# Kernel optimization log

Measured on AMD Instinct MI355X. Metric: run time of the kernel, lower is better.

## Reference

```python
import jax, jax.numpy as jnp
import numpy as np

N_NODES = 50000
N_EDGES = 800000
D_IN = 256
D_HID = 256
D_OUT = 256


def setup_inputs() -> dict:
    key = jax.random.key(0)
    ks = jax.random.split(key, 14)
    s = 1.0 / np.sqrt(D_IN)
    inp = {
        "x": jax.random.normal(ks[0], (N_NODES, D_IN), dtype=jnp.float32),
        "edge_index": jax.random.randint(ks[1], (2, N_EDGES), 0, N_NODES, dtype=jnp.int64),
        "edge_attr": jax.random.uniform(ks[2], (N_EDGES, 1), dtype=jnp.float32),
        # GCNConv layer weights (3 layers)
        "W1": jax.random.normal(ks[3], (D_IN, D_HID), dtype=jnp.float32) * s,
        "b1": jnp.zeros((D_HID,), dtype=jnp.float32),
        "W2": jax.random.normal(ks[4], (D_HID, D_HID), dtype=jnp.float32) * s,
        "b2": jnp.zeros((D_HID,), dtype=jnp.float32),
        "W3": jax.random.normal(ks[5], (D_HID, D_OUT), dtype=jnp.float32) * s,
        "b3": jnp.zeros((D_OUT,), dtype=jnp.float32),
        # edge MLP: Linear(1,8) -> ReLU -> Linear(8,1) -> Sigmoid
        "mw1": jax.random.normal(ks[6], (1, 8), dtype=jnp.float32),
        "mb1": jnp.zeros((8,), dtype=jnp.float32),
        "mw2": jax.random.normal(ks[7], (8, 1), dtype=jnp.float32) * (1.0 / np.sqrt(8.0)),
        "mb2": jnp.zeros((1,), dtype=jnp.float32),
    }
    return inp


def _gcn_layer(x, src, dst, ew, W, b, n):
    """PyG GCNConv: add self-loops (weight 1), symmetric normalization."""
    deg = jax.ops.segment_sum(ew, dst, num_segments=n) + 1.0  # self-loop contributes 1
    dinv = jax.lax.rsqrt(deg)                                 # [N]
    norm = dinv[src] * ew * dinv[dst]                         # [E]
    h = x @ W + b                                             # [N, d_out]
    agg = jax.ops.segment_sum(h[src] * norm[:, None], dst, num_segments=n)
    # self-loop term: dinv[i] * 1 * dinv[i] = 1/deg[i]
    return agg + h * (1.0 / deg)[:, None]


def reference(x, edge_index, edge_attr, W1, b1, W2, b2, W3, b3, mw1, mb1, mw2, mb2):
    src, dst = edge_index[0], edge_index[1]
    # edge weight MLP with sigmoid gate
    h = jax.nn.relu(edge_attr @ mw1 + mb1)
    ew = jax.nn.sigmoid(h @ mw2 + mb2)[:, 0]  # [E]

    n = x.shape[0]
    x = jax.nn.relu(_gcn_layer(x, src, dst, ew, W1, b1, n))  # dropout inactive (eval)
    x = jax.nn.relu(_gcn_layer(x, src, dst, ew, W2, b2, n))
    x = _gcn_layer(x, src, dst, ew, W3, b3, n)
    return x
```

## Files before the change

kernel.cpp:

```cpp
#include <hip/hip_runtime.h>
#include <hip/hip_bf16.h>
#include <stdint.h>

#define GCN_N 50000
#define GCN_E 800000
#define GCN_D 256

typedef __attribute__((ext_vector_type(8))) short bf16x8;
typedef __attribute__((ext_vector_type(4))) float f32x4;
typedef unsigned short ushort_t;
typedef unsigned long long u64;

__device__ __forceinline__ float bf2f(ushort_t u) {
    return __uint_as_float(((unsigned)u) << 16);
}
__device__ __forceinline__ ushort_t f2bf(float f) {
    unsigned v = __float_as_uint(f);
    v += 0x7FFFu + ((v >> 16) & 1u);
    return (ushort_t)(v >> 16);
}


__global__ void init_kernel(u64* dc, int n) {
    int i = blockIdx.x * blockDim.x + threadIdx.x;
    if (i < n) dc[i] = 0ull;
}

__global__ void edge_mlp_kernel(const float* __restrict__ attr,
                                const int* __restrict__ dst,
                                const float* __restrict__ mw1, const float* __restrict__ mb1,
                                const float* __restrict__ mw2, const float* __restrict__ mb2,
                                float* __restrict__ ew, u64* __restrict__ dc,
                                int* __restrict__ rank, int e_count) {
    int e = blockIdx.x * blockDim.x + threadIdx.x;
    if (e >= e_count) return;
    float a = attr[e];
    float s = mb2[0];
#pragma unroll
    for (int j = 0; j < 8; ++j) {
        float hj = fmaf(a, mw1[j], mb1[j]);
        hj = fmaxf(hj, 0.0f);
        s = fmaf(hj, mw2[j], s);
    }
    float w = 1.0f / (1.0f + expf(-s));
    ew[e] = w;
    u64 pack = (1ull << 40) + (u64)((double)w * 4294967296.0);
    u64 old = atomicAdd(&dc[dst[e]], pack);
    rank[e] = (int)(old >> 40);
}

__global__ void node_kernel(const u64* __restrict__ dc, float* __restrict__ dinv,
                            float* __restrict__ invdeg, int n) {
    int i = blockIdx.x * blockDim.x + threadIdx.x;
    if (i < n) {
        u64 v = dc[i];
        float wsum = (float)((double)(v & ((1ull << 40) - 1)) * (1.0 / 4294967296.0));
        float d = 1.0f + wsum;
        dinv[i] = rsqrtf(d);
        invdeg[i] = 1.0f / d;
    }
}

__global__ __launch_bounds__(1024) void scan1_kernel(const u64* __restrict__ dc,
                                                     int* __restrict__ part,
                                                     int* __restrict__ bsum, int n) {
    __shared__ int s[1024];
    int tid = threadIdx.x;
    int i = blockIdx.x * 1024 + tid;
    int v = (i < n) ? (int)(dc[i] >> 40) : 0;
    s[tid] = v;
    __syncthreads();
#pragma unroll
    for (int d = 1; d < 1024; d <<= 1) {
        int t = (tid >= d) ? s[tid - d] : 0;
        __syncthreads();
        s[tid] += t;
        __syncthreads();
    }
    if (i < n) part[i] = s[tid] - v;
    if (tid == 1023) bsum[blockIdx.x] = s[1023];
}

__global__ void scan2_kernel(int* bsum, int nb) {
    int t = threadIdx.x;
    int orig = (t < nb) ? bsum[t] : 0;
    int v = orig;
#pragma unroll
    for (int d = 1; d < 64; d <<= 1) {
        int u = __shfl_up(v, d, 64);
        if (t >= d) v += u;
    }
    if (t < nb) bsum[t] = v - orig;
}

__global__ void scan3_kernel(const int* __restrict__ part, const int* __restrict__ bsum,
                             int* __restrict__ offs, int n, int e_total) {
    int i = blockIdx.x * blockDim.x + threadIdx.x;
    if (i < n) offs[i] = part[i] + bsum[i >> 10];
    if (i == 0) offs[n] = e_total;
}

__global__ void scatter_kernel(const int* __restrict__ src, const int* __restrict__ dst,
                               const float* __restrict__ ew, const float* __restrict__ dinv,
                               const int* __restrict__ offs, const int* __restrict__ rank,
                               int2* __restrict__ csr, int e_count) {
    int e = blockIdx.x * blockDim.x + threadIdx.x;
    if (e >= e_count) return;
    int sN = src[e], dN = dst[e];
    int pos = offs[dN] + rank[e];
    float w = dinv[sN] * ew[e] * dinv[dN];
    csr[pos] = make_int2(sN, __float_as_int(w));
}


__global__ __launch_bounds__(256) void wconvert_kernel(const float* __restrict__ W,
                                                       ushort_t* __restrict__ wtf_hi,
                                                       ushort_t* __restrict__ wtf_lo) {
    __shared__ ushort_t lds_hi[32][256];
    __shared__ ushort_t lds_lo[32][256];
    const int kt = blockIdx.x;
    const int tid = threadIdx.x;
    for (int c = 0; c < 32; ++c) {
        float f = W[(kt * 32 + c) * GCN_D + tid];
        unsigned u = __float_as_uint(f);
        ushort_t hi = (ushort_t)(u >> 16);
        float r = f - __uint_as_float(u & 0xFFFF0000u);
        lds_hi[c][tid] = hi;
        lds_lo[c][tid] = f2bf(r);
    }
    __syncthreads();
#pragma unroll
    for (int q = 0; q < 4; ++q) {
        int slot = q * 256 + tid;
        int lane = slot & 63, nt = slot >> 6;
        int n = nt * 16 + (lane & 15);
        int kl = (lane >> 4) * 8;
        ushort_t h8[8], l8[8];
#pragma unroll
        for (int j = 0; j < 8; ++j) { h8[j] = lds_hi[kl + j][n]; l8[j] = lds_lo[kl + j][n]; }
        size_t o = ((size_t)(kt * 16 + nt) * 64 + lane) * 8;
#pragma unroll
        for (int j = 0; j < 8; ++j) { wtf_hi[o + j] = h8[j]; wtf_lo[o + j] = l8[j]; }
    }
}


__device__ __forceinline__ void split_f32x8(float4 f0, float4 f1, bf16x8& hi, bf16x8& lo) {
    float f[8] = {f0.x, f0.y, f0.z, f0.w, f1.x, f1.y, f1.z, f1.w};
#pragma unroll
    for (int i = 0; i < 8; ++i) {
        unsigned u = __float_as_uint(f[i]);
        hi[i] = (short)(u >> 16);
        float r = f[i] - __uint_as_float(u & 0xFFFF0000u);
        lo[i] = (short)f2bf(r);
    }
}

__global__ __launch_bounds__(256) void mfma_gemm_f32_kernel(
        const float* __restrict__ x,
        const ushort_t* __restrict__ wtf_hi,
        const ushort_t* __restrict__ wtf_lo,
        const float* __restrict__ bias,
        ushort_t* __restrict__ out_h,
        int n_rows) {
    __shared__ ushort_t csmem[4 * 16 * 132];
    const int lane = threadIdx.x & 63;
    const int wv   = threadIdx.x >> 6;
    const int r16  = lane & 15;
    const int kg   = lane >> 4;
    const int row0 = blockIdx.x * 32 + (wv >> 1) * 16;
    const int nt0  = (wv & 1) * 8;

    f32x4 acc[8];
#pragma unroll
    for (int nt = 0; nt < 8; ++nt) acc[nt] = (f32x4){0.f, 0.f, 0.f, 0.f};

    const int arow = row0 + r16;
    const float* ap = (arow < n_rows) ? &x[(size_t)arow * GCN_D + kg * 8] : nullptr;

#pragma unroll 1
    for (int kt = 0; kt < 8; ++kt) {
        float4 f0 = make_float4(0.f, 0.f, 0.f, 0.f), f1 = f0;
        if (ap) {
            f0 = *(const float4*)(ap + kt * 32);
            f1 = *(const float4*)(ap + kt * 32 + 4);
        }
        const bf16x8* bhp = (const bf16x8*)wtf_hi + ((size_t)kt * 16 + nt0) * 64 + lane;
        const bf16x8* blp = (const bf16x8*)wtf_lo + ((size_t)kt * 16 + nt0) * 64 + lane;
        bf16x8 bh[8], bl[8];
#pragma unroll
        for (int nt = 0; nt < 8; ++nt) bh[nt] = bhp[nt * 64];
#pragma unroll
        for (int nt = 0; nt < 8; ++nt) bl[nt] = blp[nt * 64];
        bf16x8 a_hi, a_lo;
        split_f32x8(f0, f1, a_hi, a_lo);
#pragma unroll
        for (int nt = 0; nt < 8; ++nt) {
            acc[nt] = __builtin_amdgcn_mfma_f32_16x16x32_bf16(a_hi, bh[nt], acc[nt], 0, 0, 0);
            acc[nt] = __builtin_amdgcn_mfma_f32_16x16x32_bf16(a_lo, bh[nt], acc[nt], 0, 0, 0);
            acc[nt] = __builtin_amdgcn_mfma_f32_16x16x32_bf16(a_hi, bl[nt], acc[nt], 0, 0, 0);
        }
    }

    ushort_t* my = csmem + wv * (16 * 132);
#pragma unroll
    for (int nt = 0; nt < 8; ++nt) {
        float bv = bias[(nt0 + nt) * 16 + r16];
#pragma unroll
        for (int r = 0; r < 4; ++r)
            my[(kg * 4 + r) * 132 + nt * 16 + r16] = f2bf(acc[nt][r] + bv);
    }
#pragma unroll 4
    for (int r = 0; r < 16; ++r) {
        int row = row0 + r;
        if (row < n_rows) {
            unsigned v = *(unsigned*)&my[r * 132 + lane * 2];
            *(unsigned*)&out_h[(size_t)row * GCN_D + nt0 * 16 + lane * 2] = v;
        }
    }
}


__global__ __launch_bounds__(256) void mfma_gemm_bf16_kernel(
        const ushort_t* __restrict__ a_in,
        const ushort_t* __restrict__ wtf_hi,
        const float* __restrict__ bias,
        ushort_t* __restrict__ out_h,
        int n_rows) {
    __shared__ ushort_t csmem[4 * 16 * 132];
    const int lane = threadIdx.x & 63;
    const int wv   = threadIdx.x >> 6;
    const int r16  = lane & 15;
    const int kg   = lane >> 4;
    const int row0 = blockIdx.x * 32 + (wv >> 1) * 16;
    const int nt0  = (wv & 1) * 8;

    f32x4 acc[8];
#pragma unroll
    for (int nt = 0; nt < 8; ++nt) acc[nt] = (f32x4){0.f, 0.f, 0.f, 0.f};

    const int arow = row0 + r16;
    const ushort_t* ap = (arow < n_rows) ? &a_in[(size_t)arow * GCN_D + kg * 8] : nullptr;

#pragma unroll 2
    for (int kt = 0; kt < 8; ++kt) {
        bf16x8 a = (bf16x8){0, 0, 0, 0, 0, 0, 0, 0};
        if (ap) a = *(const bf16x8*)(ap + kt * 32);
        const bf16x8* bhp = (const bf16x8*)wtf_hi + ((size_t)kt * 16 + nt0) * 64 + lane;
        bf16x8 bh[8];
#pragma unroll
        for (int nt = 0; nt < 8; ++nt) bh[nt] = bhp[nt * 64];
#pragma unroll
        for (int nt = 0; nt < 8; ++nt)
            acc[nt] = __builtin_amdgcn_mfma_f32_16x16x32_bf16(a, bh[nt], acc[nt], 0, 0, 0);
    }

    ushort_t* my = csmem + wv * (16 * 132);
#pragma unroll
    for (int nt = 0; nt < 8; ++nt) {
        float bv = bias[(nt0 + nt) * 16 + r16];
#pragma unroll
        for (int r = 0; r < 4; ++r)
            my[(kg * 4 + r) * 132 + nt * 16 + r16] = f2bf(acc[nt][r] + bv);
    }
#pragma unroll 4
    for (int r = 0; r < 16; ++r) {
        int row = row0 + r;
        if (row < n_rows) {
            unsigned v = *(unsigned*)&my[r * 132 + lane * 2];
            *(unsigned*)&out_h[(size_t)row * GCN_D + nt0 * 16 + lane * 2] = v;
        }
    }
}


template <int OUT_BF16>
__global__ __launch_bounds__(256) void spmm_kernel(const ushort_t* __restrict__ h,
                                                   const int* __restrict__ offs,
                                                   const int2* __restrict__ csr,
                                                   const float* __restrict__ invdeg,
                                                   void* __restrict__ outp, int n) {
    int wid = (blockIdx.x * blockDim.x + threadIdx.x) >> 6;
    int lane = threadIdx.x & 63;
    if (wid >= n) return;
    const ushort4* h4 = (const ushort4*)h;
    ushort4 sv = h4[(size_t)wid * 64 + lane];
    float sw = invdeg[wid];
    float4 acc;
    acc.x = bf2f(sv.x) * sw; acc.y = bf2f(sv.y) * sw;
    acc.z = bf2f(sv.z) * sw; acc.w = bf2f(sv.w) * sw;
    int e0 = offs[wid], e1 = offs[wid + 1];
    int k = e0;
    for (; k + 16 <= e1; k += 16) {
        int2 ee[16]; ushort4 vv[16];
#pragma unroll
        for (int u = 0; u < 16; ++u) ee[u] = csr[k + u];
#pragma unroll
        for (int u = 0; u < 16; ++u) vv[u] = h4[(size_t)ee[u].x * 64 + lane];
#pragma unroll
        for (int u = 0; u < 16; ++u) {
            float w = __int_as_float(ee[u].y);
            acc.x = fmaf(w, bf2f(vv[u].x), acc.x);
            acc.y = fmaf(w, bf2f(vv[u].y), acc.y);
            acc.z = fmaf(w, bf2f(vv[u].z), acc.z);
            acc.w = fmaf(w, bf2f(vv[u].w), acc.w);
        }
    }
    if (k + 8 <= e1) {
        int2 ee[8]; ushort4 vv[8];
#pragma unroll
        for (int u = 0; u < 8; ++u) ee[u] = csr[k + u];
#pragma unroll
        for (int u = 0; u < 8; ++u) vv[u] = h4[(size_t)ee[u].x * 64 + lane];
#pragma unroll
        for (int u = 0; u < 8; ++u) {
            float w = __int_as_float(ee[u].y);
            acc.x = fmaf(w, bf2f(vv[u].x), acc.x);
            acc.y = fmaf(w, bf2f(vv[u].y), acc.y);
            acc.z = fmaf(w, bf2f(vv[u].z), acc.z);
            acc.w = fmaf(w, bf2f(vv[u].w), acc.w);
        }
        k += 8;
    }
    for (; k < e1; ++k) {
        int2 e = csr[k];
        float w = __int_as_float(e.y);
        ushort4 hv = h4[(size_t)e.x * 64 + lane];
        acc.x = fmaf(w, bf2f(hv.x), acc.x);
        acc.y = fmaf(w, bf2f(hv.y), acc.y);
        acc.z = fmaf(w, bf2f(hv.z), acc.z);
        acc.w = fmaf(w, bf2f(hv.w), acc.w);
    }
    if (OUT_BF16) {
        ushort4 o;
        o.x = f2bf(fmaxf(acc.x, 0.f));
        o.y = f2bf(fmaxf(acc.y, 0.f));
        o.z = f2bf(fmaxf(acc.z, 0.f));
        o.w = f2bf(fmaxf(acc.w, 0.f));
        ((ushort4*)outp)[(size_t)wid * 64 + lane] = o;
    } else {
        ((float4*)outp)[(size_t)wid * 64 + lane] = acc;
    }
}


extern "C" void kernel_launch(void* const* d_in, const int* in_sizes, int n_in,
                              void* d_out, int out_size, void* d_ws, size_t ws_size,
                              hipStream_t stream) {
    const float* x    = (const float*)d_in[0];
    const int*   ei   = (const int*)d_in[1];
    const float* attr = (const float*)d_in[2];
    const float* W1 = (const float*)d_in[3];  const float* b1 = (const float*)d_in[4];
    const float* W2 = (const float*)d_in[5];  const float* b2 = (const float*)d_in[6];
    const float* W3 = (const float*)d_in[7];  const float* b3 = (const float*)d_in[8];
    const float* mw1 = (const float*)d_in[9]; const float* mb1 = (const float*)d_in[10];
    const float* mw2 = (const float*)d_in[11];const float* mb2 = (const float*)d_in[12];
    float* out = (float*)d_out;

    const int N = GCN_N, E = GCN_E;
    const int* srcI = ei;
    const int* dstI = ei + E;

    char* ws = (char*)d_ws;
    float* ew     = (float*)ws;                      ws += (size_t)E * 4;
    int*   rank   = (int*)ws;                        ws += (size_t)E * 4;
    u64*   dc     = (u64*)(((uintptr_t)ws + 255) & ~(uintptr_t)255); ws = (char*)(dc + N);
    float* dinv   = (float*)ws;                      ws += (size_t)N * 4;
    float* invdeg = (float*)ws;                      ws += (size_t)N * 4;
    int*   offs   = (int*)ws;                        ws += (size_t)(N + 1) * 4;
    int*   bsum   = (int*)ws;                        ws += 64 * 4;
    int*   part   = (int*)ws;                        ws += (size_t)N * 4;
    int2*  csr    = (int2*)(((uintptr_t)ws + 255) & ~(uintptr_t)255); ws = (char*)(csr + E);
    ushort_t* h   = (ushort_t*)(((uintptr_t)ws + 255) & ~(uintptr_t)255);
    ws = (char*)(h + (size_t)N * GCN_D);
    ushort_t* act = (ushort_t*)(((uintptr_t)ws + 255) & ~(uintptr_t)255);
    ws = (char*)(act + (size_t)N * GCN_D);
    ushort_t* wtf = (ushort_t*)(((uintptr_t)ws + 255) & ~(uintptr_t)255);
    ushort_t* wtf_hi1 = wtf;
    ushort_t* wtf_lo1 = wtf + 65536;
    ushort_t* wtf_hi2 = wtf + 2 * 65536;
    ushort_t* wtf_lo2 = wtf + 3 * 65536;
    ushort_t* wtf_hi3 = wtf + 4 * 65536;
    ushort_t* wtf_lo3 = wtf + 5 * 65536;

    init_kernel<<<(N + 255) / 256, 256, 0, stream>>>(dc, N);
    edge_mlp_kernel<<<(E + 255) / 256, 256, 0, stream>>>(attr, dstI, mw1, mb1, mw2, mb2,
                                                         ew, dc, rank, E);
    node_kernel<<<(N + 255) / 256, 256, 0, stream>>>(dc, dinv, invdeg, N);
    int nb = (N + 1023) / 1024;
    scan1_kernel<<<nb, 1024, 0, stream>>>(dc, part, bsum, N);
    scan2_kernel<<<1, 64, 0, stream>>>(bsum, nb);
    scan3_kernel<<<(N + 255) / 256, 256, 0, stream>>>(part, bsum, offs, N, E);
    scatter_kernel<<<(E + 255) / 256, 256, 0, stream>>>(srcI, dstI, ew, dinv, offs, rank,
                                                        csr, E);
    wconvert_kernel<<<8, 256, 0, stream>>>(W1, wtf_hi1, wtf_lo1);
    wconvert_kernel<<<8, 256, 0, stream>>>(W2, wtf_hi2, wtf_lo2);
    wconvert_kernel<<<8, 256, 0, stream>>>(W3, wtf_hi3, wtf_lo3);

    const int gemm_grid = (N + 31) / 32;
    const int spmm_grid = (N * 64 + 255) / 256;

    mfma_gemm_f32_kernel<<<gemm_grid, 256, 0, stream>>>(x, wtf_hi1, wtf_lo1, b1, h, N);
    spmm_kernel<1><<<spmm_grid, 256, 0, stream>>>(h, offs, csr, invdeg, act, N);
    mfma_gemm_bf16_kernel<<<gemm_grid, 256, 0, stream>>>(act, wtf_hi2, b2, h, N);
    spmm_kernel<1><<<spmm_grid, 256, 0, stream>>>(h, offs, csr, invdeg, act, N);
    mfma_gemm_bf16_kernel<<<gemm_grid, 256, 0, stream>>>(act, wtf_hi3, b3, h, N);
    spmm_kernel<0><<<spmm_grid, 256, 0, stream>>>(h, offs, csr, invdeg, out, N);
}
```

Before: 381.8 us.

## Stage weight tiles in LDS and give each wave all output columns

Both GEMM kernels now process 64 rows per block. Each wave computes all 256 output columns for its 16 rows, instead of two waves splitting the columns. Each K-slice of the pre-swizzled weights is loaded cooperatively into shared memory once per block and reused by all four waves, cutting redundant global/L2 weight traffic and halving A-row reloads. The cost is twice as many accumulator registers per wave, two barriers per K step, and a larger LDS footprint, which may lower occupancy.

```diff
diff --git a/kernel.cpp b/kernel.cpp
--- a/kernel.cpp
+++ b/kernel.cpp
@@ -163,20 +163,22 @@
         const float* __restrict__ bias,
         ushort_t* __restrict__ out_h,
         int n_rows) {
-    __shared__ ushort_t csmem[4 * 16 * 132];
-    const int lane = threadIdx.x & 63;
-    const int wv   = threadIdx.x >> 6;
+    __shared__ ushort_t smem[4 * 16 * 264];
+    const int tid  = threadIdx.x;
+    const int lane = tid & 63;
+    const int wv   = tid >> 6;
     const int r16  = lane & 15;
     const int kg   = lane >> 4;
-    const int row0 = blockIdx.x * 32 + (wv >> 1) * 16;
-    const int nt0  = (wv & 1) * 8;
-
-    f32x4 acc[8];
-#pragma unroll
-    for (int nt = 0; nt < 8; ++nt) acc[nt] = (f32x4){0.f, 0.f, 0.f, 0.f};
+    const int row0 = blockIdx.x * 64 + wv * 16;
+
+    f32x4 acc[16];
+#pragma unroll
+    for (int nt = 0; nt < 16; ++nt) acc[nt] = (f32x4){0.f, 0.f, 0.f, 0.f};
 
     const int arow = row0 + r16;
     const float* ap = (arow < n_rows) ? &x[(size_t)arow * GCN_D + kg * 8] : nullptr;
+    bf16x8* sH = (bf16x8*)smem;
+    bf16x8* sL = ((bf16x8*)smem) + 1024;
 
 #pragma unroll 1
     for (int kt = 0; kt < 8; ++kt) {
@@ -185,37 +187,40 @@
             f0 = *(const float4*)(ap + kt * 32);
             f1 = *(const float4*)(ap + kt * 32 + 4);
         }
-        const bf16x8* bhp = (const bf16x8*)wtf_hi + ((size_t)kt * 16 + nt0) * 64 + lane;
-        const bf16x8* blp = (const bf16x8*)wtf_lo + ((size_t)kt * 16 + nt0) * 64 + lane;
-        bf16x8 bh[8], bl[8];
-#pragma unroll
-        for (int nt = 0; nt < 8; ++nt) bh[nt] = bhp[nt * 64];
-#pragma unroll
-        for (int nt = 0; nt < 8; ++nt) bl[nt] = blp[nt * 64];
+        const bf16x8* gh = (const bf16x8*)wtf_hi + (size_t)kt * 1024;
+        const bf16x8* gl = (const bf16x8*)wtf_lo + (size_t)kt * 1024;
+        bf16x8 t0 = gh[tid], t1 = gh[256 + tid], t2 = gh[512 + tid], t3 = gh[768 + tid];
+        bf16x8 u0 = gl[tid], u1 = gl[256 + tid], u2 = gl[512 + tid], u3 = gl[768 + tid];
+        sH[tid] = t0; sH[256 + tid] = t1; sH[512 + tid] = t2; sH[768 + tid] = t3;
+        sL[tid] = u0; sL[256 + tid] = u1; sL[512 + tid] = u2; sL[768 + tid] = u3;
         bf16x8 a_hi, a_lo;
         split_f32x8(f0, f1, a_hi, a_lo);
-#pragma unroll
-        for (int nt = 0; nt < 8; ++nt) {
-            acc[nt] = __builtin_amdgcn_mfma_f32_16x16x32_bf16(a_hi, bh[nt], acc[nt], 0, 0, 0);
-            acc[nt] = __builtin_amdgcn_mfma_f32_16x16x32_bf16(a_lo, bh[nt], acc[nt], 0, 0, 0);
-            acc[nt] = __builtin_amdgcn_mfma_f32_16x16x32_bf16(a_hi, bl[nt], acc[nt], 0, 0, 0);
-        }
-    }
-
-    ushort_t* my = csmem + wv * (16 * 132);
-#pragma unroll
-    for (int nt = 0; nt < 8; ++nt) {
-        float bv = bias[(nt0 + nt) * 16 + r16];
+        __syncthreads();
+#pragma unroll
+        for (int nt = 0; nt < 16; ++nt) {
+            bf16x8 bh = sH[nt * 64 + lane];
+            bf16x8 bl = sL[nt * 64 + lane];
+            acc[nt] = __builtin_amdgcn_mfma_f32_16x16x32_bf16(a_hi, bh, acc[nt], 0, 0, 0);
+            acc[nt] = __builtin_amdgcn_mfma_f32_16x16x32_bf16(a_lo, bh, acc[nt], 0, 0, 0);
+            acc[nt] = __builtin_amdgcn_mfma_f32_16x16x32_bf16(a_hi, bl, acc[nt], 0, 0, 0);
+        }
+        __syncthreads();
+    }
+
+    ushort_t* my = smem + wv * (16 * 264);
+#pragma unroll
+    for (int nt = 0; nt < 16; ++nt) {
+        float bv = bias[nt * 16 + r16];
 #pragma unroll
         for (int r = 0; r < 4; ++r)
-            my[(kg * 4 + r) * 132 + nt * 16 + r16] = f2bf(acc[nt][r] + bv);
+            my[(kg * 4 + r) * 264 + nt * 16 + r16] = f2bf(acc[nt][r] + bv);
     }
 #pragma unroll 4
     for (int r = 0; r < 16; ++r) {
         int row = row0 + r;
         if (row < n_rows) {
-            unsigned v = *(unsigned*)&my[r * 132 + lane * 2];
-            *(unsigned*)&out_h[(size_t)row * GCN_D + nt0 * 16 + lane * 2] = v;
+            ushort4 v = *(ushort4*)&my[r * 264 + lane * 4];
+            *(ushort4*)&out_h[(size_t)row * GCN_D + lane * 4] = v;
         }
     }
 }
@@ -227,48 +232,52 @@
         const float* __restrict__ bias,
         ushort_t* __restrict__ out_h,
         int n_rows) {
-    __shared__ ushort_t csmem[4 * 16 * 132];
-    const int lane = threadIdx.x & 63;
-    const int wv   = threadIdx.x >> 6;
+    __shared__ ushort_t smem[4 * 16 * 264];
+    const int tid  = threadIdx.x;
+    const int lane = tid & 63;
+    const int wv   = tid >> 6;
     const int r16  = lane & 15;
     const int kg   = lane >> 4;
-    const int row0 = blockIdx.x * 32 + (wv >> 1) * 16;
-    const int nt0  = (wv & 1) * 8;
-
-    f32x4 acc[8];
-#pragma unroll
-    for (int nt = 0; nt < 8; ++nt) acc[nt] = (f32x4){0.f, 0.f, 0.f, 0.f};
+    const int row0 = blockIdx.x * 64 + wv * 16;
+
+    f32x4 acc[16];
+#pragma unroll
+    for (int nt = 0; nt < 16; ++nt) acc[nt] = (f32x4){0.f, 0.f, 0.f, 0.f};
 
     const int arow = row0 + r16;
     const ushort_t* ap = (arow < n_rows) ? &a_in[(size_t)arow * GCN_D + kg * 8] : nullptr;
-
-#pragma unroll 2
+    bf16x8* sH = (bf16x8*)smem;
+
+#pragma unroll 1
     for (int kt = 0; kt < 8; ++kt) {
         bf16x8 a = (bf16x8){0, 0, 0, 0, 0, 0, 0, 0};
         if (ap) a = *(const bf16x8*)(ap + kt * 32);
-        const bf16x8* bhp = (const bf16x8*)wtf_hi + ((size_t)kt * 16 + nt0) * 64 + lane;
-        bf16x8 bh[8];
-#pragma unroll
-        for (int nt = 0; nt < 8; ++nt) bh[nt] = bhp[nt * 64];
-#pragma unroll
-        for (int nt = 0; nt < 8; ++nt)
-            acc[nt] = __builtin_amdgcn_mfma_f32_16x16x32_bf16(a, bh[nt], acc[nt], 0, 0, 0);
-    }
-
-    ushort_t* my = csmem + wv * (16 * 132);
-#pragma unroll
-    for (int nt = 0; nt < 8; ++nt) {
-        float bv = bias[(nt0 + nt) * 16 + r16];
+        const bf16x8* gh = (const bf16x8*)wtf_hi + (size_t)kt * 1024;
+        bf16x8 t0 = gh[tid], t1 = gh[256 + tid], t2 = gh[512 + tid], t3 = gh[768 + tid];
+        sH[tid] = t0; sH[256 + tid] = t1; sH[512 + tid] = t2; sH[768 + tid] = t3;
+        __syncthreads();
+#pragma unroll
+        for (int nt = 0; nt < 16; ++nt) {
+            bf16x8 bh = sH[nt * 64 + lane];
+            acc[nt] = __builtin_amdgcn_mfma_f32_16x16x32_bf16(a, bh, acc[nt], 0, 0, 0);
+        }
+        __syncthreads();
+    }
+
+    ushort_t* my = smem + wv * (16 * 264);
+#pragma unroll
+    for (int nt = 0; nt < 16; ++nt) {
+        float bv = bias[nt * 16 + r16];
 #pragma unroll
         for (int r = 0; r < 4; ++r)
-            my[(kg * 4 + r) * 132 + nt * 16 + r16] = f2bf(acc[nt][r] + bv);
+            my[(kg * 4 + r) * 264 + nt * 16 + r16] = f2bf(acc[nt][r] + bv);
     }
 #pragma unroll 4
     for (int r = 0; r < 16; ++r) {
         int row = row0 + r;
         if (row < n_rows) {
-            unsigned v = *(unsigned*)&my[r * 132 + lane * 2];
-            *(unsigned*)&out_h[(size_t)row * GCN_D + nt0 * 16 + lane * 2] = v;
+            ushort4 v = *(ushort4*)&my[r * 264 + lane * 4];
+            *(ushort4*)&out_h[(size_t)row * GCN_D + lane * 4] = v;
         }
     }
 }
@@ -397,7 +406,7 @@
     wconvert_kernel<<<8, 256, 0, stream>>>(W2, wtf_hi2, wtf_lo2);
     wconvert_kernel<<<8, 256, 0, stream>>>(W3, wtf_hi3, wtf_lo3);
 
-    const int gemm_grid = (N + 31) / 32;
+    const int gemm_grid = (N + 63) / 64;
     const int spmm_grid = (N * 64 + 255) / 256;
 
     mfma_gemm_f32_kernel<<<gemm_grid, 256, 0, stream>>>(x, wtf_hi1, wtf_lo1, b1, h, N);
```

After: 356.3 us. -6.7%, faster.
